# Kernel tuning notes

Measured on AMD Instinct MI355X. Metric: run time of the kernel, lower is better.

## Reference

```python
import jax, jax.numpy as jnp
import numpy as np

D_MODEL = 1024
D_K = 1024
D_V = 1024
B = 4
S = 4096


def apply_rope(x, cos, sin):
    # x: [B, S, D]; cos/sin: [S, D//2] (broadcast over batch)
    d_half = x.shape[-1] // 2
    x0, x1 = x[..., :d_half], x[..., d_half:]
    return jnp.concatenate([x0 * cos - x1 * sin, x0 * sin + x1 * cos], axis=-1)


def setup_inputs() -> dict:
    key = jax.random.key(0)
    ks = jax.random.split(key, 9)
    x = jax.random.normal(ks[0], (B, S, D_MODEL), dtype=jnp.float32)
    cos = jax.random.uniform(ks[1], (S, D_K // 2), dtype=jnp.float32)
    sin = jax.random.uniform(ks[2], (S, D_K // 2), dtype=jnp.float32)
    # nn.Linear params: weight [out, in], bias [out]
    sq = 1.0 / np.sqrt(D_MODEL)
    W_q = jax.random.uniform(ks[3], (D_K, D_MODEL), minval=-sq, maxval=sq)
    b_q = jax.random.uniform(ks[4], (D_K,), minval=-sq, maxval=sq)
    W_k = jax.random.uniform(ks[5], (D_K, D_MODEL), minval=-sq, maxval=sq)
    b_k = jax.random.uniform(ks[6], (D_K,), minval=-sq, maxval=sq)
    W_v = jax.random.uniform(ks[7], (D_V, D_MODEL), minval=-sq, maxval=sq)
    b_v = jax.random.uniform(ks[8], (D_V,), minval=-sq, maxval=sq)
    return {"x": x, "cos": cos, "sin": sin, "W_q": W_q, "b_q": b_q,
            "W_k": W_k, "b_k": b_k, "W_v": W_v, "b_v": b_v}


def reference(x, cos, sin, W_q, b_q, W_k, b_k, W_v, b_v):
    seq_len = x.shape[1]
    Q = jnp.einsum('bsm,km->bsk', x, W_q) + b_q
    K = jnp.einsum('bsm,km->bsk', x, W_k) + b_k
    Q = apply_rope(Q, cos, sin)
    K = apply_rope(K, cos, sin)
    scores = jnp.einsum('bqk,btk->bqt', Q, K) / jnp.sqrt(jnp.float32(D_K))
    causal = jnp.tril(jnp.ones((seq_len, seq_len), dtype=bool))  # [S, S]
    scores = jnp.where(causal, scores, -jnp.inf)
    attn = jax.nn.softmax(scores, axis=-1)
    V = jnp.einsum('bsm,vm->bsv', x, W_v) + b_v
    z = jnp.einsum('bqt,btv->bqv', attn, V)
    return z
```

## Files before the change

### kernel.cpp

```cpp
#include <hip/hip_runtime.h>
#include <cstdint>
#include <cstddef>

using short8   = __attribute__((ext_vector_type(8))) short;
using f32x4    = __attribute__((ext_vector_type(4))) float;
using ushort4v = __attribute__((ext_vector_type(4))) unsigned short;

#define DEV static __device__ __forceinline__

constexpr int NB  = 4;
constexpr int SEQ = 4096;
constexpr int DM  = 1024;
constexpr int BSR = NB * SEQ;
constexpr size_t PBSTR = 136ULL * 65536;

DEV unsigned short f2bf(float f) {
  union { float f; unsigned u; } v; v.f = f;
  unsigned r = v.u + 0x7FFFu + ((v.u >> 16) & 1u);
  return (unsigned short)(r >> 16);
}

DEV int tri(int t) { return t * (t + 1) / 2; }

DEV void gload_lds16(const void* g, void* l) {
  __builtin_amdgcn_global_load_lds(
      (__attribute__((address_space(1))) void*)(g),
      (__attribute__((address_space(3))) void*)(l), 16, 0, 0);
}

DEV f32x4 mfma16(short8 a, short8 b, f32x4 c) {
  return __builtin_amdgcn_mfma_f32_16x16x32_bf16(a, b, c, 0, 0, 0);
}

template <int N> DEV void waitvm() {
  static_assert(N == 8 || N == 10, "unsupported vmcnt");
  if constexpr (N == 8)  asm volatile("s_waitcnt vmcnt(8)" ::: "memory");
  if constexpr (N == 10) asm volatile("s_waitcnt vmcnt(10)" ::: "memory");
}
DEV void bar() { asm volatile("s_barrier" ::: "memory"); }

DEV int orig_row(int p) {
  int gI = p >> 5, rr = p & 31;
  return (rr < 16) ? (gI * 16 + rr) : (512 + gI * 16 + (rr - 16));
}

__global__ __launch_bounds__(256) void convert_kernel(
    const float* __restrict__ x,
    const float* __restrict__ Wq, const float* __restrict__ Wk, const float* __restrict__ Wv,
    const float* __restrict__ bq, const float* __restrict__ bk, const float* __restrict__ bv,
    unsigned short* __restrict__ xbf,
    unsigned short* __restrict__ Wqp, unsigned short* __restrict__ Wkp, unsigned short* __restrict__ Wvp,
    float* __restrict__ bqp, float* __restrict__ bkp, float* __restrict__ bvp)
{
  const int U1 = BSR * DM / 8;
  const int U2 = 2 * DM * DM / 8;
  const int U3 = DM * DM / 8;
  const int U4 = 3 * DM / 8;
  const int total = U1 + U2 + U3 + U4;
  for (int u = blockIdx.x * blockDim.x + threadIdx.x; u < total;
       u += gridDim.x * blockDim.x) {
    if (u < U1) {
      int e = u * 8;
      float4 f0 = ((const float4*)(x + e))[0];
      float4 f1 = ((const float4*)(x + e))[1];
      short8 o;
      o[0]=(short)f2bf(f0.x); o[1]=(short)f2bf(f0.y); o[2]=(short)f2bf(f0.z); o[3]=(short)f2bf(f0.w);
      o[4]=(short)f2bf(f1.x); o[5]=(short)f2bf(f1.y); o[6]=(short)f2bf(f1.z); o[7]=(short)f2bf(f1.w);
      *(short8*)(xbf + e) = o;
    } else if (u < U1 + U2) {
      int w = u - U1;
      int which = w >> 17;
      int r = w & (131072 - 1);
      int p = r >> 7;
      int m8 = (r & 127) * 8;
      const float* src = (which ? Wk : Wq) + (size_t)orig_row(p) * DM + m8;
      unsigned short* dst = (which ? Wkp : Wqp) + (size_t)p * DM + m8;
      float4 f0 = ((const float4*)src)[0];
      float4 f1 = ((const float4*)src)[1];
      short8 o;
      o[0]=(short)f2bf(f0.x); o[1]=(short)f2bf(f0.y); o[2]=(short)f2bf(f0.z); o[3]=(short)f2bf(f0.w);
      o[4]=(short)f2bf(f1.x); o[5]=(short)f2bf(f1.y); o[6]=(short)f2bf(f1.z); o[7]=(short)f2bf(f1.w);
      *(short8*)dst = o;
    } else if (u < U1 + U2 + U3) {
      int r = u - (U1 + U2);
      int p = r >> 7;
      int m8 = (r & 127) * 8;
      const float* src = Wv + (size_t)p * DM + m8;
      float4 f0 = ((const float4*)src)[0];
      float4 f1 = ((const float4*)src)[1];
      short8 o;
      o[0]=(short)f2bf(f0.x); o[1]=(short)f2bf(f0.y); o[2]=(short)f2bf(f0.z); o[3]=(short)f2bf(f0.w);
      o[4]=(short)f2bf(f1.x); o[5]=(short)f2bf(f1.y); o[6]=(short)f2bf(f1.z); o[7]=(short)f2bf(f1.w);
      *(short8*)(Wvp + (size_t)p * DM + m8) = o;
    } else {
      int t = u - (U1 + U2 + U3);
      int which = t >> 7;
      int i0 = (t & 127) * 8;
      for (int e = 0; e < 8; ++e) {
        int p = i0 + e;
        if (which == 0)      bqp[p] = bq[orig_row(p)];
        else if (which == 1) bkp[p] = bk[orig_row(p)];
        else                 bvp[p] = bv[p];
      }
    }
  }
}

template <int CN>
DEV void stage(const unsigned short* g, size_t ld, size_t k0,
               unsigned short* ldst, int sdst, int srow, int scg8) {
  #pragma unroll
  for (int cc = 0; cc < CN; ++cc)
    gload_lds16(g + (size_t)(cc * 128 + srow) * ld + k0 + scg8,
                (void*)(ldst + cc * 4096 + sdst));
}

template <int AROWS, int BROWS, int MF, int NF>
DEV void run_gemm(unsigned short* lds,
                  const unsigned short* __restrict__ Ag, size_t lda,
                  const unsigned short* __restrict__ Bg, size_t ldb,
                  int NT, int tid, int lane, int wm, int wn,
                  f32x4 (&acc)[MF][NF])
{
  constexpr int CA = AROWS / 128, CB = BROWS / 128;
  constexpr int VM = 2 * (CA + CB) + CA;
  constexpr int BUFE = (AROWS + BROWS) * 32;
  const int srow = tid >> 2;
  const int scg8 = (((tid & 3) ^ ((srow >> 1) & 3))) * 8;
  const int sdst = srow * 32 + (tid & 3) * 8;
  const int c = lane & 15, g = lane >> 4;
  const int gsw = (g ^ ((c >> 1) & 3)) * 8;
  int aoff[MF], boff[NF];
  #pragma unroll
  for (int f = 0; f < MF; ++f) aoff[f] = (wm * (MF * 16) + f * 16 + c) * 32 + gsw;
  #pragma unroll
  for (int f = 0; f < NF; ++f) boff[f] = AROWS * 32 + (wn * (NF * 16) + f * 16 + c) * 32 + gsw;

  #pragma unroll
  for (int p = 0; p < 3; ++p) {
    stage<CA>(Ag, lda, (size_t)p * 32, lds + p * BUFE, sdst, srow, scg8);
    stage<CB>(Bg, ldb, (size_t)p * 32, lds + p * BUFE + AROWS * 32, sdst, srow, scg8);
  }

  for (int t = 0; t < NT; ++t) {
    const int bsel = t & 3, nsel = (t + 3) & 3;
    const int ts = (t + 3 < NT) ? (t + 3) : (NT - 1);
    unsigned short* lb = lds + bsel * BUFE;
    stage<CA>(Ag, lda, (size_t)ts * 32, lds + nsel * BUFE, sdst, srow, scg8);
    waitvm<VM>();
    bar();
    short8 av[MF / 2], bv[NF];
    #pragma unroll
    for (int f = 0; f < MF / 2; ++f) av[f] = *(const short8*)(lb + aoff[f]);
    #pragma unroll
    for (int f = 0; f < NF; ++f)     bv[f] = *(const short8*)(lb + boff[f]);
    __builtin_amdgcn_s_setprio(1);
    #pragma unroll
    for (int mf = 0; mf < MF / 2; ++mf)
      #pragma unroll
      for (int nf = 0; nf < NF; ++nf)
        acc[mf][nf] = mfma16(av[mf], bv[nf], acc[mf][nf]);
    __builtin_amdgcn_s_setprio(0);
    stage<CB>(Bg, ldb, (size_t)ts * 32, lds + nsel * BUFE + AROWS * 32, sdst, srow, scg8);
    #pragma unroll
    for (int f = 0; f < MF / 2; ++f) av[f] = *(const short8*)(lb + aoff[MF / 2 + f]);
    __builtin_amdgcn_s_setprio(1);
    #pragma unroll
    for (int mf = 0; mf < MF / 2; ++mf)
      #pragma unroll
      for (int nf = 0; nf < NF; ++nf)
        acc[MF / 2 + mf][nf] = mfma16(av[mf], bv[nf], acc[MF / 2 + mf][nf]);
    __builtin_amdgcn_s_setprio(0);
    __builtin_amdgcn_sched_barrier(0);
    bar();
  }
  asm volatile("s_waitcnt vmcnt(0)" ::: "memory");
}

template <int MODE>
__global__ __launch_bounds__(512, 2) void k_gemm256(
    const unsigned short* __restrict__ Ain,
    const unsigned short* __restrict__ Bin,
    const float* __restrict__ bias,
    const float* __restrict__ cosT, const float* __restrict__ sinT,
    unsigned short* __restrict__ out, int b0, int G)
{
  __shared__ unsigned short lds[4 * 16384];
  const int tid = threadIdx.x, lane = tid & 63, wid = tid >> 6;
  const int wm = wid >> 2, wn = wid & 3;
  const int c = lane & 15, g = lane >> 4;

  const unsigned short* Ag;
  const unsigned short* Bg;
  int bm, bn, tm = 0, li = 0;
  if (MODE == 2) {
    int lin = (blockIdx.x & 7) * (17 * G) + (blockIdx.x >> 3);
    li = lin / 136;
    int t136 = lin - li * 136;
    tm = (int)((sqrtf(8.0f * (float)t136 + 1.0f) - 1.0f) * 0.5f);
    while (tri(tm + 1) <= t136) ++tm;
    while (tri(tm) > t136) --tm;
    int tn = t136 - tri(tm);
    int b = b0 + li;
    bm = tm * 256; bn = tn * 256;
    Ag = Ain + ((size_t)b * SEQ + bm) * DM;
    Bg = Bin + ((size_t)b * SEQ + bn) * DM;
  } else {
    int xcd = blockIdx.x & 7, idx = blockIdx.x >> 3;
    bm = (xcd * 8 + (idx >> 2)) * 256;
    bn = (idx & 3) * 256;
    Ag = Ain + (size_t)bm * DM;
    Bg = Bin + (size_t)bn * DM;
  }

  f32x4 z4 = {0.f, 0.f, 0.f, 0.f};
  f32x4 acc[8][4];
  #pragma unroll
  for (int m = 0; m < 8; ++m)
    #pragma unroll
    for (int n = 0; n < 4; ++n) acc[m][n] = z4;

  run_gemm<256, 256, 8, 4>(lds, Ag, DM, Bg, DM, 32, tid, lane, wm, wn, acc);

  if (MODE == 0) {
    #pragma unroll
    for (int am = 0; am < 8; ++am) {
      int row0 = bm + wm * 128 + am * 16 + g * 4;
      #pragma unroll
      for (int fp = 0; fp < 4; fp += 2) {
        int f_g = (bn >> 4) + wn * 4 + fp;
        float b0f = bias[f_g * 16 + c];
        float b1f = bias[f_g * 16 + 16 + c];
        int j = (f_g >> 1) * 16 + c;
        #pragma unroll
        for (int r = 0; r < 4; ++r) {
          int rowg = row0 + r;
          int s = rowg & (SEQ - 1);
          float x0 = acc[am][fp][r] + b0f;
          float x1 = acc[am][fp + 1][r] + b1f;
          float cv = cosT[(size_t)s * (DM / 2) + j];
          float sv = sinT[(size_t)s * (DM / 2) + j];
          out[(size_t)rowg * DM + f_g * 16 + c]      = f2bf(x0 * cv - x1 * sv);
          out[(size_t)rowg * DM + f_g * 16 + 16 + c] = f2bf(x0 * sv + x1 * cv);
        }
      }
    }
  } else if (MODE == 1) {
    #pragma unroll
    for (int am = 0; am < 8; ++am) {
      int s0 = bm + wm * 128 + am * 16 + g * 4;
      int bb = s0 >> 12;
      int sl = s0 & (SEQ - 1);
      #pragma unroll
      for (int fn = 0; fn < 4; ++fn) {
        int v = bn + wn * 64 + fn * 16 + c;
        float bv_ = bias[v];
        ushort4v pk;
        #pragma unroll
        for (int r = 0; r < 4; ++r) pk[r] = f2bf(acc[am][fn][r] + bv_);
        *(ushort4v*)(out + ((size_t)(bb * DM + v)) * SEQ + sl) = pk;
      }
    }
  } else {
    const size_t Kp = (size_t)(tm + 1) * 256;
    unsigned short* pb = out + (size_t)li * PBSTR + (size_t)tri(tm) * 65536;
    #pragma unroll
    for (int am = 0; am < 8; ++am) {
      int lrow = wm * 128 + am * 16 + g * 4;
      #pragma unroll
      for (int fn = 0; fn < 4; ++fn) {
        int col = bn + wn * 64 + fn * 16 + c;
        #pragma unroll
        for (int r = 0; r < 4; ++r) {
          union { _Float16 h; unsigned short u; } cv;
          cv.h = (_Float16)acc[am][fn][r];
          pb[(size_t)(lrow + r) * Kp + col] = cv.u;
        }
      }
    }
  }
}

__global__ __launch_bounds__(256) void softmax_panel(unsigned short* __restrict__ S_)
{
  const int tid = threadIdx.x, wid = tid >> 6, lane = tid & 63;
  const int widx = blockIdx.x * 4 + wid;
  const int li = widx >> 12;
  const int r = widx & (SEQ - 1);
  const int p = r >> 8;
  const size_t Kp = (size_t)(p + 1) * 256;
  const int nt = (p + 1) * 2;
  unsigned short* base = S_ + (size_t)li * PBSTR + (size_t)tri(p) * 65536 +
                         (size_t)(r & 255) * Kp;
  const float K2 = 0.04508422002778011f;

  float v0[32], v1[32];
  float mx = -3.0e38f;
  #pragma unroll
  for (int tn = 0; tn < 32; ++tn) {
    if (tn < nt) {
      unsigned u = *(const unsigned*)(base + tn * 128 + lane * 2);
      union { unsigned u; _Float16 h[2]; } cv; cv.u = u;
      int col = tn * 128 + lane * 2;
      float a0 = (col     <= r) ? (float)cv.h[0] : -3.0e38f;
      float a1 = (col + 1 <= r) ? (float)cv.h[1] : -3.0e38f;
      v0[tn] = a0; v1[tn] = a1;
      mx = fmaxf(mx, fmaxf(a0, a1));
    }
  }
  #pragma unroll
  for (int d = 1; d < 64; d <<= 1) mx = fmaxf(mx, __shfl_xor(mx, d, 64));
  float sum = 0.f;
  #pragma unroll
  for (int tn = 0; tn < 32; ++tn) {
    if (tn < nt) {
      float p0 = (v0[tn] < -1.0e37f) ? 0.f : exp2f((v0[tn] - mx) * K2);
      float p1 = (v1[tn] < -1.0e37f) ? 0.f : exp2f((v1[tn] - mx) * K2);
      v0[tn] = p0; v1[tn] = p1;
      sum += p0 + p1;
    }
  }
  #pragma unroll
  for (int d = 1; d < 64; d <<= 1) sum += __shfl_xor(sum, d, 64);
  float inv = 1.0f / sum;
  #pragma unroll
  for (int tn = 0; tn < 32; ++tn) {
    if (tn < nt) {
      unsigned o = (unsigned)f2bf(v0[tn] * inv) | ((unsigned)f2bf(v1[tn] * inv) << 16);
      *(unsigned*)(base + tn * 128 + lane * 2) = o;
    }
  }
}

__global__ __launch_bounds__(512, 2) void k_pv(
    const unsigned short* __restrict__ P,
    const unsigned short* __restrict__ Vt,
    float* __restrict__ z, int b0, int G)
{
  __shared__ unsigned short lds[4 * 12288];
  const int tid = threadIdx.x, lane = tid & 63, wid = tid >> 6;
  const int wm = wid >> 1, wn = wid & 1;
  const int c = lane & 15, g = lane >> 4;
  const int x = blockIdx.x & 7;
  const int j = blockIdx.x >> 3;
  const int jid = x * G + (j >> 3);
  const int n8 = j & 7;
  const int li = jid >> 3;
  const int pl = jid & 7;
  const int b = b0 + li;
  const unsigned short* Bg = Vt + ((size_t)b * DM + n8 * 128) * SEQ;

  for (int h = 0; h < 2; ++h) {
    const int p = h ? (15 - pl) : pl;
    const int NT = (p + 1) * 8;
    const size_t Kp = (size_t)(p + 1) * 256;
    const unsigned short* panel = P + (size_t)li * PBSTR + (size_t)tri(p) * 65536;

    f32x4 z4 = {0.f, 0.f, 0.f, 0.f};
    f32x4 acc[4][4];
    #pragma unroll
    for (int m = 0; m < 4; ++m)
      #pragma unroll
      for (int n = 0; n < 4; ++n) acc[m][n] = z4;

    run_gemm<256, 128, 4, 4>(lds, panel, Kp, Bg, SEQ, NT, tid, lane, wm, wn, acc);

    #pragma unroll
    for (int am = 0; am < 4; ++am) {
      int row = p * 256 + wm * 64 + am * 16 + g * 4;
      #pragma unroll
      for (int fn = 0; fn < 4; ++fn) {
        int col = n8 * 128 + wn * 64 + fn * 16 + c;
        #pragma unroll
        for (int r = 0; r < 4; ++r)
          z[((size_t)(b * SEQ + row + r)) * DM + col] = acc[am][fn][r];
      }
    }
    __syncthreads();
  }
}

extern "C" void kernel_launch(void* const* d_in, const int* in_sizes, int n_in,
                              void* d_out, int out_size, void* d_ws, size_t ws_size,
                              hipStream_t stream) {
  const float* x    = (const float*)d_in[0];
  const float* cosT = (const float*)d_in[1];
  const float* sinT = (const float*)d_in[2];
  const float* Wq   = (const float*)d_in[3];
  const float* bq   = (const float*)d_in[4];
  const float* Wk   = (const float*)d_in[5];
  const float* bk   = (const float*)d_in[6];
  const float* Wv   = (const float*)d_in[7];
  const float* bv   = (const float*)d_in[8];
  float* z = (float*)d_out;

  char* ws = (char*)d_ws;
  unsigned short* xbf = (unsigned short*)(ws);
  unsigned short* Wqp = (unsigned short*)(ws + 33554432);
  unsigned short* Wkp = (unsigned short*)(ws + 35651584);
  unsigned short* Wvp = (unsigned short*)(ws + 37748736);
  float* bqp = (float*)(ws + 39845888);
  float* bkp = (float*)(ws + 39849984);
  float* bvp = (float*)(ws + 39854080);
  unsigned short* Qbf = (unsigned short*)(ws + 39858176);
  unsigned short* Kbf = (unsigned short*)(ws + 73412608);
  unsigned short* Vtb = (unsigned short*)(ws + 106967040);
  const size_t BASE = 140521472ULL;
  const size_t PER  = PBSTR * 2ULL;
  unsigned short* Sc = (unsigned short*)(ws + BASE);

  int G = 1;
  if (ws_size >= BASE + 4 * PER)      G = 4;
  else if (ws_size >= BASE + 2 * PER) G = 2;

  convert_kernel<<<dim3(2048), dim3(256), 0, stream>>>(
      x, Wq, Wk, Wv, bq, bk, bv, xbf, Wqp, Wkp, Wvp, bqp, bkp, bvp);

  k_gemm256<0><<<dim3(256), dim3(512), 0, stream>>>(xbf, Wqp, bqp, cosT, sinT, Qbf, 0, 1);
  k_gemm256<0><<<dim3(256), dim3(512), 0, stream>>>(xbf, Wkp, bkp, cosT, sinT, Kbf, 0, 1);
  k_gemm256<1><<<dim3(256), dim3(512), 0, stream>>>(xbf, Wvp, bvp, cosT, sinT, Vtb, 0, 1);

  for (int b0 = 0; b0 < NB; b0 += G) {
    k_gemm256<2><<<dim3(136 * G), dim3(512), 0, stream>>>(Qbf, Kbf, nullptr, nullptr, nullptr, Sc, b0, G);
    softmax_panel<<<dim3(1024 * G), dim3(256), 0, stream>>>(Sc);
    k_pv<<<dim3(64 * G), dim3(512), 0, stream>>>(Sc, Vtb, z, b0, G);
  }
}
```

Before: 371.4 us.

## Split GEMM k-step into four phases interleaving loads, barriers and MFMAs

Restructures the inner GEMM loop so each k-step runs in four phases. Each phase issues one global-to-LDS load, reads a quarter of the A fragments and runs the matching MFMA block, with barriers between phases. This is a ping-pong style schedule meant to spread memory traffic across the compute and keep the wave groups interleaved. The vmcnt wait is recomputed for the new load order. The extra barriers and full lgkmcnt waits per phase add synchronisation overhead, and the code assumes CA is 2 and MF is divisible by 4.

```diff
diff --git a/kernel.cpp b/kernel.cpp
--- a/kernel.cpp
+++ b/kernel.cpp
@@ -33,9 +33,9 @@
 }
 
 template <int N> DEV void waitvm() {
-  static_assert(N == 8 || N == 10, "unsupported vmcnt");
-  if constexpr (N == 8)  asm volatile("s_waitcnt vmcnt(8)" ::: "memory");
-  if constexpr (N == 10) asm volatile("s_waitcnt vmcnt(10)" ::: "memory");
+  static_assert(N == 7 || N == 9, "unsupported vmcnt");
+  if constexpr (N == 7) asm volatile("s_waitcnt vmcnt(7)" ::: "memory");
+  if constexpr (N == 9) asm volatile("s_waitcnt vmcnt(9)" ::: "memory");
 }
 DEV void bar() { asm volatile("s_barrier" ::: "memory"); }
 
@@ -123,8 +123,10 @@
                   f32x4 (&acc)[MF][NF])
 {
   constexpr int CA = AROWS / 128, CB = BROWS / 128;
-  constexpr int VM = 2 * (CA + CB) + CA;
+  constexpr int LPT = CA + CB;
+  constexpr int VM = 2 * LPT + 1;
   constexpr int BUFE = (AROWS + BROWS) * 32;
+  constexpr int MPP = MF / 4;
   const int srow = tid >> 2;
   const int scg8 = (((tid & 3) ^ ((srow >> 1) & 3))) * 8;
   const int sdst = srow * 32 + (tid & 3) * 8;
@@ -143,36 +145,46 @@
   }
 
   for (int t = 0; t < NT; ++t) {
-    const int bsel = t & 3, nsel = (t + 3) & 3;
-    const int ts = (t + 3 < NT) ? (t + 3) : (NT - 1);
-    unsigned short* lb = lds + bsel * BUFE;
-    stage<CA>(Ag, lda, (size_t)ts * 32, lds + nsel * BUFE, sdst, srow, scg8);
-    waitvm<VM>();
-    bar();
-    short8 av[MF / 2], bv[NF];
-    #pragma unroll
-    for (int f = 0; f < MF / 2; ++f) av[f] = *(const short8*)(lb + aoff[f]);
-    #pragma unroll
-    for (int f = 0; f < NF; ++f)     bv[f] = *(const short8*)(lb + boff[f]);
-    __builtin_amdgcn_s_setprio(1);
-    #pragma unroll
-    for (int mf = 0; mf < MF / 2; ++mf)
-      #pragma unroll
-      for (int nf = 0; nf < NF; ++nf)
-        acc[mf][nf] = mfma16(av[mf], bv[nf], acc[mf][nf]);
-    __builtin_amdgcn_s_setprio(0);
-    stage<CB>(Bg, ldb, (size_t)ts * 32, lds + nsel * BUFE + AROWS * 32, sdst, srow, scg8);
-    #pragma unroll
-    for (int f = 0; f < MF / 2; ++f) av[f] = *(const short8*)(lb + aoff[MF / 2 + f]);
-    __builtin_amdgcn_s_setprio(1);
-    #pragma unroll
-    for (int mf = 0; mf < MF / 2; ++mf)
-      #pragma unroll
-      for (int nf = 0; nf < NF; ++nf)
-        acc[MF / 2 + mf][nf] = mfma16(av[mf], bv[nf], acc[MF / 2 + mf][nf]);
-    __builtin_amdgcn_s_setprio(0);
-    __builtin_amdgcn_sched_barrier(0);
-    bar();
+    unsigned short* lb = lds + (t & 3) * BUFE;
+    unsigned short* nb = lds + ((t + 3) & 3) * BUFE;
+    const size_t ts = (t + 3 < NT) ? (size_t)(t + 3) : (size_t)(NT - 1);
+    short8 bvv[NF];
+    #pragma unroll
+    for (int ph = 0; ph < 4; ++ph) {
+      if (ph == 0)
+        gload_lds16(Ag + (size_t)srow * lda + ts * 32 + scg8, (void*)(nb + sdst));
+      else if (ph == 1)
+        gload_lds16(Ag + (size_t)(128 + srow) * lda + ts * 32 + scg8, (void*)(nb + 4096 + sdst));
+      else if (ph == 2)
+        gload_lds16(Bg + (size_t)srow * ldb + ts * 32 + scg8, (void*)(nb + AROWS * 32 + sdst));
+      else if (CB == 2)
+        gload_lds16(Bg + (size_t)(128 + srow) * ldb + ts * 32 + scg8, (void*)(nb + AROWS * 32 + 4096 + sdst));
+
+      short8 av[MPP];
+      if (ph == 0) {
+        waitvm<VM>();
+        bar();
+        #pragma unroll
+        for (int f = 0; f < MPP; ++f) av[f] = *(const short8*)(lb + aoff[f]);
+        #pragma unroll
+        for (int f = 0; f < NF; ++f) bvv[f] = *(const short8*)(lb + boff[f]);
+      } else {
+        #pragma unroll
+        for (int f = 0; f < MPP; ++f) av[f] = *(const short8*)(lb + aoff[ph * MPP + f]);
+        bar();
+      }
+      asm volatile("s_waitcnt lgkmcnt(0)" ::: "memory");
+      __builtin_amdgcn_sched_barrier(0);
+      __builtin_amdgcn_s_setprio(1);
+      #pragma unroll
+      for (int mf = 0; mf < MPP; ++mf)
+        #pragma unroll
+        for (int nf = 0; nf < NF; ++nf)
+          acc[ph * MPP + mf][nf] = mfma16(av[mf], bvv[nf], acc[ph * MPP + mf][nf]);
+      __builtin_amdgcn_s_setprio(0);
+      __builtin_amdgcn_sched_barrier(0);
+      bar();
+    }
   }
   asm volatile("s_waitcnt vmcnt(0)" ::: "memory");
 }
```

Result: slower. 379.1 us (+2.1%).

## Rewrite 256x256 GEMM main loop as 8-phase fine-grained LDS pipeline

Applied to the files above, without the earlier changes.

Replaces the generic 4-buffer K-loop used by the projection and score GEMMs with a hand-scheduled 8-phase loop. Each phase issues two global-to-LDS loads, reads one half of the A fragments, and runs 16 MFMAs between barriers, over two 64-wide K double buffers. The goal is to interleave loads with compute more finely and hide memory latency behind MFMA work. The row mapping changes to wm*128 + mh*64, so the epilogues are adjusted to match. The PV GEMM keeps the old scheme as a specialised copy. The change adds more barriers per K step and relies on hand-tuned vmcnt values that must exactly match the number of loads in flight.

```diff
diff --git a/kernel.cpp b/kernel.cpp
--- a/kernel.cpp
+++ b/kernel.cpp
@@ -32,11 +32,6 @@
   return __builtin_amdgcn_mfma_f32_16x16x32_bf16(a, b, c, 0, 0, 0);
 }
 
-template <int N> DEV void waitvm() {
-  static_assert(N == 8 || N == 10, "unsupported vmcnt");
-  if constexpr (N == 8)  asm volatile("s_waitcnt vmcnt(8)" ::: "memory");
-  if constexpr (N == 10) asm volatile("s_waitcnt vmcnt(10)" ::: "memory");
-}
 DEV void bar() { asm volatile("s_barrier" ::: "memory"); }
 
 DEV int orig_row(int p) {
@@ -106,73 +101,94 @@
   }
 }
 
-template <int CN>
-DEV void stage(const unsigned short* g, size_t ld, size_t k0,
-               unsigned short* ldst, int sdst, int srow, int scg8) {
-  #pragma unroll
-  for (int cc = 0; cc < CN; ++cc)
-    gload_lds16(g + (size_t)(cc * 128 + srow) * ld + k0 + scg8,
-                (void*)(ldst + cc * 4096 + sdst));
-}
-
-template <int AROWS, int BROWS, int MF, int NF>
-DEV void run_gemm(unsigned short* lds,
-                  const unsigned short* __restrict__ Ag, size_t lda,
-                  const unsigned short* __restrict__ Bg, size_t ldb,
-                  int NT, int tid, int lane, int wm, int wn,
-                  f32x4 (&acc)[MF][NF])
-{
-  constexpr int CA = AROWS / 128, CB = BROWS / 128;
-  constexpr int VM = 2 * (CA + CB) + CA;
-  constexpr int BUFE = (AROWS + BROWS) * 32;
-  const int srow = tid >> 2;
-  const int scg8 = (((tid & 3) ^ ((srow >> 1) & 3))) * 8;
-  const int sdst = srow * 32 + (tid & 3) * 8;
+
+template <int DB, int MH, int KS, bool RB, int SREG, bool DOVM>
+DEV void phase8(unsigned short* lds, const unsigned short* SG, int scol,
+                const int (&aoff)[2][4], const int (&boff)[4], int tid,
+                short8 (&bv)[4], f32x4 (&acc)[8][4])
+{
+  if (DOVM) asm volatile("s_waitcnt vmcnt(6)" ::: "memory");
+  gload_lds16(SG + (size_t)(tid >> 2) * 1024 + scol,
+              (void*)(lds + SREG + tid * 8));
+  gload_lds16(SG + (size_t)((tid >> 2) + 128) * 1024 + scol,
+              (void*)(lds + SREG + 4096 + tid * 8));
+  short8 av[4];
+  #pragma unroll
+  for (int f = 0; f < 4; ++f)
+    av[f] = *(const short8*)(lds + DB + KS * 8192 + aoff[MH][f]);
+  if (RB) {
+    #pragma unroll
+    for (int f = 0; f < 4; ++f)
+      bv[f] = *(const short8*)(lds + DB + 16384 + KS * 8192 + boff[f]);
+  }
+  bar();
+  asm volatile("s_waitcnt lgkmcnt(0)" ::: "memory");
+  __builtin_amdgcn_sched_barrier(0);
+  __builtin_amdgcn_s_setprio(1);
+  #pragma unroll
+  for (int fm = 0; fm < 4; ++fm)
+    #pragma unroll
+    for (int fn = 0; fn < 4; ++fn)
+      acc[MH * 4 + fm][fn] = mfma16(av[fm], bv[fn], acc[MH * 4 + fm][fn]);
+  __builtin_amdgcn_s_setprio(0);
+  __builtin_amdgcn_sched_barrier(0);
+  bar();
+}
+
+DEV void run_gemm8(unsigned short* lds,
+                   const unsigned short* __restrict__ Ag,
+                   const unsigned short* __restrict__ Bg,
+                   int tid, int lane, int wm, int wn,
+                   f32x4 (&acc)[8][4])
+{
   const int c = lane & 15, g = lane >> 4;
   const int gsw = (g ^ ((c >> 1) & 3)) * 8;
-  int aoff[MF], boff[NF];
-  #pragma unroll
-  for (int f = 0; f < MF; ++f) aoff[f] = (wm * (MF * 16) + f * 16 + c) * 32 + gsw;
-  #pragma unroll
-  for (int f = 0; f < NF; ++f) boff[f] = AROWS * 32 + (wn * (NF * 16) + f * 16 + c) * 32 + gsw;
-
-  #pragma unroll
-  for (int p = 0; p < 3; ++p) {
-    stage<CA>(Ag, lda, (size_t)p * 32, lds + p * BUFE, sdst, srow, scg8);
-    stage<CB>(Bg, ldb, (size_t)p * 32, lds + p * BUFE + AROWS * 32, sdst, srow, scg8);
-  }
-
-  for (int t = 0; t < NT; ++t) {
-    const int bsel = t & 3, nsel = (t + 3) & 3;
-    const int ts = (t + 3 < NT) ? (t + 3) : (NT - 1);
-    unsigned short* lb = lds + bsel * BUFE;
-    stage<CA>(Ag, lda, (size_t)ts * 32, lds + nsel * BUFE, sdst, srow, scg8);
-    waitvm<VM>();
-    bar();
-    short8 av[MF / 2], bv[NF];
-    #pragma unroll
-    for (int f = 0; f < MF / 2; ++f) av[f] = *(const short8*)(lb + aoff[f]);
-    #pragma unroll
-    for (int f = 0; f < NF; ++f)     bv[f] = *(const short8*)(lb + boff[f]);
-    __builtin_amdgcn_s_setprio(1);
-    #pragma unroll
-    for (int mf = 0; mf < MF / 2; ++mf)
-      #pragma unroll
-      for (int nf = 0; nf < NF; ++nf)
-        acc[mf][nf] = mfma16(av[mf], bv[nf], acc[mf][nf]);
-    __builtin_amdgcn_s_setprio(0);
-    stage<CB>(Bg, ldb, (size_t)ts * 32, lds + nsel * BUFE + AROWS * 32, sdst, srow, scg8);
-    #pragma unroll
-    for (int f = 0; f < MF / 2; ++f) av[f] = *(const short8*)(lb + aoff[MF / 2 + f]);
-    __builtin_amdgcn_s_setprio(1);
-    #pragma unroll
-    for (int mf = 0; mf < MF / 2; ++mf)
-      #pragma unroll
-      for (int nf = 0; nf < NF; ++nf)
-        acc[MF / 2 + mf][nf] = mfma16(av[mf], bv[nf], acc[MF / 2 + mf][nf]);
-    __builtin_amdgcn_s_setprio(0);
-    __builtin_amdgcn_sched_barrier(0);
-    bar();
+  const int scg = (((tid & 3) ^ ((tid >> 3) & 3))) * 8;
+  int aoff[2][4], boff[4];
+  #pragma unroll
+  for (int mh = 0; mh < 2; ++mh)
+    #pragma unroll
+    for (int f = 0; f < 4; ++f)
+      aoff[mh][f] = (wm * 128 + mh * 64 + f * 16 + c) * 32 + gsw;
+  #pragma unroll
+  for (int f = 0; f < 4; ++f)
+    boff[f] = (wn * 64 + f * 16 + c) * 32 + gsw;
+
+  {
+    const int r0 = tid >> 2;
+    gload_lds16(Ag + (size_t)r0 * 1024 + scg,              (void*)(lds + tid * 8));
+    gload_lds16(Ag + (size_t)(r0 + 128) * 1024 + scg,      (void*)(lds + 4096 + tid * 8));
+    gload_lds16(Bg + (size_t)r0 * 1024 + scg,              (void*)(lds + 16384 + tid * 8));
+    gload_lds16(Bg + (size_t)(r0 + 128) * 1024 + scg,      (void*)(lds + 16384 + 4096 + tid * 8));
+    gload_lds16(Ag + (size_t)r0 * 1024 + 32 + scg,         (void*)(lds + 8192 + tid * 8));
+    gload_lds16(Ag + (size_t)(r0 + 128) * 1024 + 32 + scg, (void*)(lds + 8192 + 4096 + tid * 8));
+    gload_lds16(Bg + (size_t)r0 * 1024 + 32 + scg,         (void*)(lds + 24576 + tid * 8));
+    gload_lds16(Bg + (size_t)(r0 + 128) * 1024 + 32 + scg, (void*)(lds + 24576 + 4096 + tid * 8));
+    gload_lds16(Ag + (size_t)r0 * 1024 + 64 + scg,         (void*)(lds + 32768 + tid * 8));
+    gload_lds16(Ag + (size_t)(r0 + 128) * 1024 + 64 + scg, (void*)(lds + 32768 + 4096 + tid * 8));
+    gload_lds16(Bg + (size_t)r0 * 1024 + 64 + scg,         (void*)(lds + 49152 + tid * 8));
+    gload_lds16(Bg + (size_t)(r0 + 128) * 1024 + 64 + scg, (void*)(lds + 49152 + 4096 + tid * 8));
+  }
+  asm volatile("s_waitcnt vmcnt(4)" ::: "memory");
+  bar();
+
+  short8 bv[4];
+  for (int it = 0; it < 8; ++it) {
+    const int s1 = 2 * it + 1;
+    const int s2 = (2 * it + 2 < 16) ? 2 * it + 2 : 15;
+    const int s3 = (2 * it + 3 < 16) ? 2 * it + 3 : 15;
+    const int c1  = s1 * 64 + 32 + scg;
+    const int c2a = s2 * 64 + scg;
+    const int c2b = s2 * 64 + 32 + scg;
+    const int c3  = s3 * 64 + scg;
+    phase8<0,     0, 0, true,  40960, false>(lds, Ag, c1,  aoff, boff, tid, bv, acc);
+    phase8<0,     1, 0, false, 57344, true >(lds, Bg, c1,  aoff, boff, tid, bv, acc);
+    phase8<0,     0, 1, true,  0,     false>(lds, Ag, c2a, aoff, boff, tid, bv, acc);
+    phase8<0,     1, 1, false, 16384, true >(lds, Bg, c2a, aoff, boff, tid, bv, acc);
+    phase8<32768, 0, 0, true,  8192,  false>(lds, Ag, c2b, aoff, boff, tid, bv, acc);
+    phase8<32768, 1, 0, false, 24576, true >(lds, Bg, c2b, aoff, boff, tid, bv, acc);
+    phase8<32768, 0, 1, true,  32768, false>(lds, Ag, c3,  aoff, boff, tid, bv, acc);
+    phase8<32768, 1, 1, false, 49152, true >(lds, Bg, c3,  aoff, boff, tid, bv, acc);
   }
   asm volatile("s_waitcnt vmcnt(0)" ::: "memory");
 }
@@ -185,7 +201,7 @@
     const float* __restrict__ cosT, const float* __restrict__ sinT,
     unsigned short* __restrict__ out, int b0, int G)
 {
-  __shared__ unsigned short lds[4 * 16384];
+  __shared__ unsigned short lds[65536];
   const int tid = threadIdx.x, lane = tid & 63, wid = tid >> 6;
   const int wm = wid >> 2, wn = wid & 3;
   const int c = lane & 15, g = lane >> 4;
@@ -220,12 +236,12 @@
     #pragma unroll
     for (int n = 0; n < 4; ++n) acc[m][n] = z4;
 
-  run_gemm<256, 256, 8, 4>(lds, Ag, DM, Bg, DM, 32, tid, lane, wm, wn, acc);
+  run_gemm8(lds, Ag, Bg, tid, lane, wm, wn, acc);
 
   if (MODE == 0) {
     #pragma unroll
     for (int am = 0; am < 8; ++am) {
-      int row0 = bm + wm * 128 + am * 16 + g * 4;
+      int row0 = bm + wm * 128 + (am >> 2) * 64 + (am & 3) * 16 + g * 4;
       #pragma unroll
       for (int fp = 0; fp < 4; fp += 2) {
         int f_g = (bn >> 4) + wn * 4 + fp;
@@ -248,7 +264,7 @@
   } else if (MODE == 1) {
     #pragma unroll
     for (int am = 0; am < 8; ++am) {
-      int s0 = bm + wm * 128 + am * 16 + g * 4;
+      int s0 = bm + wm * 128 + (am >> 2) * 64 + (am & 3) * 16 + g * 4;
       int bb = s0 >> 12;
       int sl = s0 & (SEQ - 1);
       #pragma unroll
@@ -266,7 +282,7 @@
     unsigned short* pb = out + (size_t)li * PBSTR + (size_t)tri(tm) * 65536;
     #pragma unroll
     for (int am = 0; am < 8; ++am) {
-      int lrow = wm * 128 + am * 16 + g * 4;
+      int lrow = wm * 128 + (am >> 2) * 64 + (am & 3) * 16 + g * 4;
       #pragma unroll
       for (int fn = 0; fn < 4; ++fn) {
         int col = bn + wn * 64 + fn * 16 + c;
@@ -330,6 +346,74 @@
       *(unsigned*)(base + tn * 128 + lane * 2) = o;
     }
   }
+}
+
+template <int CN>
+DEV void stage_pv(const unsigned short* g, size_t ld, size_t k0,
+                  unsigned short* ldst, int sdst, int srow, int scg8) {
+  #pragma unroll
+  for (int cc = 0; cc < CN; ++cc)
+    gload_lds16(g + (size_t)(cc * 128 + srow) * ld + k0 + scg8,
+                (void*)(ldst + cc * 4096 + sdst));
+}
+
+DEV void run_gemm_pv(unsigned short* lds,
+                     const unsigned short* __restrict__ Ag, size_t lda,
+                     const unsigned short* __restrict__ Bg, size_t ldb,
+                     int NT, int tid, int lane, int wm, int wn,
+                     f32x4 (&acc)[4][4])
+{
+  constexpr int BUFE = (256 + 128) * 32;
+  const int srow = tid >> 2;
+  const int scg8 = (((tid & 3) ^ ((srow >> 1) & 3))) * 8;
+  const int sdst = srow * 32 + (tid & 3) * 8;
+  const int c = lane & 15, g = lane >> 4;
+  const int gsw = (g ^ ((c >> 1) & 3)) * 8;
+  int aoff[4], boff[4];
+  #pragma unroll
+  for (int f = 0; f < 4; ++f) aoff[f] = (wm * 64 + f * 16 + c) * 32 + gsw;
+  #pragma unroll
+  for (int f = 0; f < 4; ++f) boff[f] = 256 * 32 + (wn * 64 + f * 16 + c) * 32 + gsw;
+
+  #pragma unroll
+  for (int p = 0; p < 3; ++p) {
+    stage_pv<2>(Ag, lda, (size_t)p * 32, lds + p * BUFE, sdst, srow, scg8);
+    stage_pv<1>(Bg, ldb, (size_t)p * 32, lds + p * BUFE + 256 * 32, sdst, srow, scg8);
+  }
+
+  for (int t = 0; t < NT; ++t) {
+    const int bsel = t & 3, nsel = (t + 3) & 3;
+    const size_t ts = (size_t)((t + 3 < NT) ? t + 3 : NT - 1);
+    unsigned short* lb = lds + bsel * BUFE;
+    stage_pv<2>(Ag, lda, ts * 32, lds + nsel * BUFE, sdst, srow, scg8);
+    asm volatile("s_waitcnt vmcnt(7)" ::: "memory");
+    bar();
+    short8 av[2], bv[4];
+    #pragma unroll
+    for (int f = 0; f < 2; ++f) av[f] = *(const short8*)(lb + aoff[f]);
+    #pragma unroll
+    for (int f = 0; f < 4; ++f) bv[f] = *(const short8*)(lb + boff[f]);
+    __builtin_amdgcn_s_setprio(1);
+    #pragma unroll
+    for (int mf = 0; mf < 2; ++mf)
+      #pragma unroll
+      for (int nf = 0; nf < 4; ++nf)
+        acc[mf][nf] = mfma16(av[mf], bv[nf], acc[mf][nf]);
+    __builtin_amdgcn_s_setprio(0);
+    stage_pv<1>(Bg, ldb, ts * 32, lds + nsel * BUFE + 256 * 32, sdst, srow, scg8);
+    #pragma unroll
+    for (int f = 0; f < 2; ++f) av[f] = *(const short8*)(lb + aoff[2 + f]);
+    __builtin_amdgcn_s_setprio(1);
+    #pragma unroll
+    for (int mf = 0; mf < 2; ++mf)
+      #pragma unroll
+      for (int nf = 0; nf < 4; ++nf)
+        acc[2 + mf][nf] = mfma16(av[mf], bv[nf], acc[2 + mf][nf]);
+    __builtin_amdgcn_s_setprio(0);
+    __builtin_amdgcn_sched_barrier(0);
+    bar();
+  }
+  asm volatile("s_waitcnt vmcnt(0)" ::: "memory");
 }
 
 __global__ __launch_bounds__(512, 2) void k_pv(
@@ -363,7 +447,7 @@
       #pragma unroll
       for (int n = 0; n < 4; ++n) acc[m][n] = z4;
 
-    run_gemm<256, 128, 4, 4>(lds, panel, Kp, Bg, SEQ, NT, tid, lane, wm, wn, acc);
+    run_gemm_pv(lds, panel, Kp, Bg, SEQ, NT, tid, lane, wm, wn, acc);
 
     #pragma unroll
     for (int am = 0; am < 4; ++am) {
```

Measured after the change: 356.2 us. 4.1% less time.
